# Performance work log

Hardware: AMD Instinct MI355X
Metric: run time of the kernel (lower is better)

Reference implementation:

```python
import jax, jax.numpy as jnp
import numpy as np

LN_EPS = 1e-5
TOP_K = 2

def _layer_norm(x, g, b):
    m = jnp.mean(x, axis=-1, keepdims=True)
    v = jnp.var(x, axis=-1, keepdims=True)
    return (x - m) * jax.lax.rsqrt(v + LN_EPS) * g + b

def _skew(X, pad_value):
    # shift every row one step right: [B,M,L] -> [B,M,M+L]
    B, M, L = X.shape
    X = jnp.pad(X, ((0, 0), (0, 0), (0, M + 1)), constant_values=pad_value)
    X = X.reshape(B, -1)[:, :-M]
    return X.reshape(B, M, M + L)

def _unskew(X):
    # reverse of _skew: [B,M,M+L] -> [B,M,L]
    B, M, Lt = X.shape
    L = Lt - M
    X = X.reshape(B, -1)
    X = jnp.pad(X, ((0, 0), (0, M)))
    return X.reshape(B, M, M + L + 1)[:, :, :L]

def _heads(x, K, D):
    # [B,T,H] -> [B*K,T,D]
    B, T, _ = x.shape
    return x.reshape(B, T, K, D).transpose(0, 2, 1, 3).reshape(B * K, T, D)

def setup_inputs() -> dict:
    key = jax.random.key(0)
    ks = jax.random.split(key, 12)
    B, M, L, H, Dh, E, Kh = 4, 512, 512, 1024, 2048, 8, 8
    D = H // Kh
    s = 0.02
    return {
        "h": jax.random.normal(ks[0], (B, M, H), jnp.float32),
        "h_cache": jax.random.normal(ks[1], (B, L, H), jnp.float32),
        "key_pe": jax.random.normal(ks[2], (1, D, L), jnp.float32) * s,
        "Wq": jax.random.normal(ks[3], (H, H), jnp.float32) * s,
        "Wk": jax.random.normal(ks[4], (H, H), jnp.float32) * s,
        "Wv": jax.random.normal(ks[5], (H, H), jnp.float32) * s,
        "Wo": jax.random.normal(ks[6], (H, H), jnp.float32) * s,
        "ln1_g": jnp.ones((H,), jnp.float32),
        "ln1_b": jnp.zeros((H,), jnp.float32),
        "gate_W": jax.random.normal(ks[7], (H, E), jnp.float32) * s,
        "gate_b": jnp.zeros((E,), jnp.float32),
        "W1": jax.random.normal(ks[8], (E, H, Dh), jnp.float32) * s,
        "b1": jnp.zeros((E, Dh), jnp.float32),
        "W2": jax.random.normal(ks[9], (E, Dh, H), jnp.float32) * s,
        "b2": jnp.zeros((E, H), jnp.float32),
        "ln2_g": jnp.ones((H,), jnp.float32),
        "ln2_b": jnp.zeros((H,), jnp.float32),
    }

def reference(h, h_cache, key_pe, Wq, Wk, Wv, Wo, ln1_g, ln1_b,
              gate_W, gate_b, W1, b1, W2, b2, ln2_g, ln2_b):
    B, M, H = h.shape
    L = h_cache.shape[1]
    Kh = 8
    D = H // Kh
    # --- multi-head relative-position attention over (cache, current) ---
    h_all = jnp.concatenate([h_cache, h], axis=1)            # [B, L+M, H]
    q = _heads(h @ Wq, Kh, D)                                # [B*K, M, D]
    k = _heads(h_all @ Wk, Kh, D)                            # [B*K, M+L, D]
    v = _heads(h_all @ Wv, Kh, D)                            # [B*K, M+L, D]
    attn_cont = _unskew(jnp.einsum('bmd,bnd->bmn', q, k))    # [B*K, M, L]
    attn_pos = jnp.einsum('bmd,xdl->bml', q, key_pe)         # [B*K, M, L]
    attn = jax.nn.softmax((attn_cont + attn_pos) / jnp.sqrt(jnp.float32(D)), axis=-1)
    out = jnp.einsum('bmn,bnd->bmd', _skew(attn, 0.0), v)    # [B*K, M, D]
    out = out.reshape(B, Kh, M, D).transpose(0, 2, 1, 3).reshape(B, M, H)
    attn_out = out @ Wo
    h1 = _layer_norm(h + attn_out, ln1_g, ln1_b)             # post-LN residual
    # --- top-k gated MoE FFN (NaiveGate), post-LN residual ---
    x = h1.reshape(-1, H)                                    # [N, H]
    N = x.shape[0]
    E = gate_b.shape[0]
    logits = x @ gate_W + gate_b                             # [N, E]
    top_val, top_idx = jax.lax.top_k(logits, TOP_K)          # [N, k]
    scores = jax.nn.softmax(top_val, axis=-1)                # [N, k]
    combine = jnp.zeros((N, E), x.dtype).at[jnp.arange(N)[:, None], top_idx].add(scores)
    he = jax.nn.relu(jnp.einsum('nh,ehf->enf', x, W1) + b1[:, None, :])  # [E, N, Dh]
    ye = jnp.einsum('enf,efh->enh', he, W2) + b2[:, None, :]             # [E, N, H]
    core = jnp.einsum('ne,enh->nh', combine, ye).reshape(B, M, H)
    output = _layer_norm(h1 + core, ln2_g, ln2_b)
    return output, top_idx
```

## Files before the change

### kernel.cpp

```cpp
#include <hip/hip_runtime.h>
#include <hip/hip_bf16.h>
#include <stdint.h>


typedef _Float16 f16;
typedef _Float16 f16x8 __attribute__((ext_vector_type(8)));
typedef _Float16 f16x4 __attribute__((ext_vector_type(4)));
typedef float    f32x4 __attribute__((ext_vector_type(4)));
typedef int      i32x4 __attribute__((ext_vector_type(4)));

#define MFMA16(a, b, c) __builtin_amdgcn_mfma_f32_16x16x32_f16((a), (b), (c), 0, 0, 0)
#define LO_SCALE 2048.0f
#define LO_INV   4.8828125e-4f

__device__ __forceinline__ void split2(float x, f16* h, f16* l) {
  f16 hh = (f16)x;
  *h = hh;
  *l = (f16)((x - (float)hh) * LO_SCALE);
}

__device__ __forceinline__ f32x4 zero4() {
  f32x4 z; z[0] = 0.f; z[1] = 0.f; z[2] = 0.f; z[3] = 0.f; return z;
}

__device__ __forceinline__ void gload_lds16(const void* g, void* l) {
  __builtin_amdgcn_global_load_lds((__attribute__((address_space(1))) void*)g,
                                   (__attribute__((address_space(3))) void*)l,
                                   16, 0, 0);
}

__global__ void __launch_bounds__(256) cast_hall_k(const float* __restrict__ h,
                                                   const float* __restrict__ hc,
                                                   f16* __restrict__ hi,
                                                   f16* __restrict__ lo) {
  int c = blockIdx.x * 256 + threadIdx.x;
  int e0 = c * 8;
  int row = e0 >> 10;
  int col = e0 & 1023;
  int b = row >> 10, pos = row & 1023;
  const float* src = (pos < 512) ? (hc + (size_t)((b << 9) + pos) * 1024 + col)
                                 : (h  + (size_t)((b << 9) + (pos - 512)) * 1024 + col);
  float4 v0 = ((const float4*)src)[0];
  float4 v1 = ((const float4*)src)[1];
  float xs[8] = {v0.x, v0.y, v0.z, v0.w, v1.x, v1.y, v1.z, v1.w};
  f16x8 vh, vl;
#pragma unroll
  for (int i = 0; i < 8; i++) { f16 a, bb; split2(xs[i], &a, &bb); vh[i] = a; vl[i] = bb; }
  *(f16x8*)&hi[e0] = vh;
  *(f16x8*)&lo[e0] = vl;
}

template <int SPLIT>
__global__ void __launch_bounds__(256) transpose_cast_k(const float* __restrict__ in,
                                                        f16* __restrict__ oh,
                                                        f16* __restrict__ ol,
                                                        int R, int C) {
  in += (size_t)blockIdx.z * R * C;
  oh += (size_t)blockIdx.z * R * C;
  if constexpr (SPLIT) ol += (size_t)blockIdx.z * R * C;
  __shared__ float tile[32][33];
  int c0 = blockIdx.x * 32, r0 = blockIdx.y * 32;
  int tr = threadIdx.x >> 3, tc = (threadIdx.x & 7) * 4;
  float4 v = *(const float4*)&in[(size_t)(r0 + tr) * C + c0 + tc];
  tile[tr][tc + 0] = v.x; tile[tr][tc + 1] = v.y; tile[tr][tc + 2] = v.z; tile[tr][tc + 3] = v.w;
  __syncthreads();
  int oc = tr;
  int orr = tc;
  f16x4 vh, vl;
#pragma unroll
  for (int i = 0; i < 4; i++) {
    float x = tile[orr + i][oc];
    f16 a, bb; split2(x, &a, &bb);
    vh[i] = a; vl[i] = bb;
  }
  *(f16x4*)&oh[(size_t)(c0 + oc) * R + r0 + orr] = vh;
  if constexpr (SPLIT) *(f16x4*)&ol[(size_t)(c0 + oc) * R + r0 + orr] = vl;
}

#define AM_ID 0
#define AM_GA 2
#define AM_PA 3
#define EP_QKV 0
#define EP_F32 2
#define EP_HE 3
#define EP_YE 4

template <int SPLIT, int BM, int BN, int AMAP, int EPI>
__global__ void __launch_bounds__(256) gemm_k(
    const f16* __restrict__ Ah, const f16* __restrict__ Al,
    const f16* __restrict__ Bh, const f16* __restrict__ Bl,
    void* __restrict__ o0, void* __restrict__ o1,
    const float* __restrict__ bias,
    int Kd, int strideA, int bExpStride,
    const int* __restrict__ list, const int* __restrict__ bases,
    const int* __restrict__ counts) {
  constexpr int PL = SPLIT ? 2 : 1;
  constexpr int MT = BM / 32;
  constexpr int NT = BN / 32;
  constexpr int AIT = BM / 64;
  constexpr int BIT = BN / 64;
  const int e = blockIdx.z;
  int cnt = 0, base0 = 0;
  if constexpr (AMAP == AM_GA || AMAP == AM_PA) {
    cnt = counts[e]; base0 = bases[e];
    if ((int)blockIdx.y * BM >= cnt) return;
    Bh += (size_t)e * bExpStride;
  }
  __shared__ f16 sA[PL][BM * 32];
  __shared__ f16 sB[PL][BN * 32];
  const int n0 = blockIdx.x * BN, r0 = blockIdx.y * BM;
  const int tid = threadIdx.x, lane = tid & 63, wv = tid >> 6;
  const int wm = (wv >> 1) * (BM / 2), wn = (wv & 1) * (BN / 2);

  f32x4 accM[MT][NT], accC[MT][NT];
#pragma unroll
  for (int i = 0; i < MT; i++)
#pragma unroll
    for (int j = 0; j < NT; j++) { accM[i][j] = zero4(); accC[i][j] = zero4(); }

  int aRow[AIT], aCu[AIT];
#pragma unroll
  for (int c = 0; c < AIT; c++) {
    int u = c * 256 + tid;
    int r = u >> 2, cu = u & 3;
    aCu[c] = ((cu ^ ((r >> 1) & 3)) << 3);
    int rr = r0 + r;
    int g;
    if constexpr (AMAP == AM_ID) g = rr;
    else if constexpr (AMAP == AM_GA) g = (rr < cnt) ? list[base0 + rr] : 0;
    else g = base0 + rr;
    aRow[c] = g;
  }
  int bRow[BIT], bCu[BIT];
#pragma unroll
  for (int c = 0; c < BIT; c++) {
    int u = c * 256 + tid;
    int r = u >> 2, cu = u & 3;
    bCu[c] = ((cu ^ ((r >> 1) & 3)) << 3);
    bRow[c] = n0 + r;
  }

  for (int k0 = 0; k0 < Kd; k0 += 32) {
#pragma unroll
    for (int c = 0; c < AIT; c++) {
      int u = c * 256 + tid;
      gload_lds16(&Ah[(size_t)aRow[c] * strideA + k0 + aCu[c]], &sA[0][u * 8]);
      if constexpr (SPLIT)
        gload_lds16(&Al[(size_t)aRow[c] * strideA + k0 + aCu[c]], &sA[1][u * 8]);
    }
#pragma unroll
    for (int c = 0; c < BIT; c++) {
      int u = c * 256 + tid;
      gload_lds16(&Bh[(size_t)bRow[c] * Kd + k0 + bCu[c]], &sB[0][u * 8]);
      if constexpr (SPLIT)
        gload_lds16(&Bl[(size_t)bRow[c] * Kd + k0 + bCu[c]], &sB[1][u * 8]);
    }
    __syncthreads();

    f16x8 ah[MT], al[MT];
#pragma unroll
    for (int mt = 0; mt < MT; mt++) {
      int r = wm + mt * 16 + (lane & 15);
      int cu = (lane >> 4) ^ ((r >> 1) & 3);
      ah[mt] = *(const f16x8*)&sA[0][(r * 4 + cu) * 8];
      if constexpr (SPLIT) al[mt] = *(const f16x8*)&sA[1][(r * 4 + cu) * 8];
    }
#pragma unroll
    for (int nt = 0; nt < NT; nt++) {
      int r = wn + nt * 16 + (lane & 15);
      int cu = (lane >> 4) ^ ((r >> 1) & 3);
      f16x8 bh = *(const f16x8*)&sB[0][(r * 4 + cu) * 8];
      f16x8 bl;
      if constexpr (SPLIT) bl = *(const f16x8*)&sB[1][(r * 4 + cu) * 8];
#pragma unroll
      for (int mt = 0; mt < MT; mt++) {
        accM[mt][nt] = MFMA16(ah[mt], bh, accM[mt][nt]);
        if constexpr (SPLIT) {
          accC[mt][nt] = MFMA16(ah[mt], bl, accC[mt][nt]);
          accC[mt][nt] = MFMA16(al[mt], bh, accC[mt][nt]);
        }
      }
    }
    __syncthreads();
  }

#pragma unroll
  for (int mt = 0; mt < MT; mt++)
#pragma unroll
    for (int nt = 0; nt < NT; nt++)
#pragma unroll
      for (int rg = 0; rg < 4; rg++) {
        int row = r0 + wm + mt * 16 + ((lane >> 4) << 2) + rg;
        int col = n0 + wn + nt * 16 + (lane & 15);
        float v = accM[mt][nt][rg];
        if constexpr (SPLIT) v += accC[mt][nt][rg] * LO_INV;
        if constexpr (EPI == EP_QKV) {
          f16* QH = (f16*)o0;
          f16* QL = QH + (1u << 21);
          f16* KH = QL + (1u << 21);
          f16* KL = KH + (1u << 22);
          f16* VTH = KL + (1u << 22);
          f16* VTL = VTH + (1u << 22);
          int b = row >> 10, pos = row & 1023;
          int seg = col >> 10, hd = (col >> 7) & 7, d = col & 127;
          f16 hh, ll; split2(v, &hh, &ll);
          if (seg == 0) {
            if (pos >= 512) {
              size_t ad = ((size_t)((((b << 3) + hd) << 9) + (pos - 512))) * 128 + d;
              QH[ad] = hh; QL[ad] = ll;
            }
          } else if (seg == 1) {
            size_t ad = ((size_t)((((b << 3) + hd) << 10) + pos)) * 128 + d;
            KH[ad] = hh; KL[ad] = ll;
          } else {
            size_t ad = ((size_t)((((b << 3) + hd) << 7) + d)) * 1024 + pos;
            VTH[ad] = hh; VTL[ad] = ll;
          }
        } else if constexpr (EPI == EP_F32) {
          ((float*)o0)[(size_t)row * 1024 + col] = v;
        } else if constexpr (EPI == EP_HE) {
          if (row < cnt) {
            float t = v + bias[(e << 11) + col];
            ((f16*)o0)[(size_t)(base0 + row) * 2048 + col] = (f16)fmaxf(t, 0.f);
          }
        } else if constexpr (EPI == EP_YE) {
          if (row < cnt)
            ((float*)o0)[(size_t)(base0 + row) * 1024 + col] = v + bias[(e << 10) + col];
        }
      }
}

__device__ __forceinline__ void unpack_p(const unsigned* sp, f16x8* hi, f16x8* lo) {
  i32x4 u0 = *(const i32x4*)sp;
  i32x4 u1 = *(const i32x4*)(sp + 4);
  i32x4 h, l;
  h[0] = (u0[0] & 0xffff) | (u0[1] << 16);
  h[1] = (u0[2] & 0xffff) | (u0[3] << 16);
  h[2] = (u1[0] & 0xffff) | (u1[1] << 16);
  h[3] = (u1[2] & 0xffff) | (u1[3] << 16);
  l[0] = (int)(((unsigned)u0[0] >> 16) | ((unsigned)u0[1] & 0xffff0000u));
  l[1] = (int)(((unsigned)u0[2] >> 16) | ((unsigned)u0[3] & 0xffff0000u));
  l[2] = (int)(((unsigned)u1[0] >> 16) | ((unsigned)u1[1] & 0xffff0000u));
  l[3] = (int)(((unsigned)u1[2] >> 16) | ((unsigned)u1[3] & 0xffff0000u));
  *hi = __builtin_bit_cast(f16x8, h);
  *lo = __builtin_bit_cast(f16x8, l);
}

__global__ void __launch_bounds__(256) attn_k(
    const f16* __restrict__ qh_, const f16* __restrict__ ql_,
    const f16* __restrict__ kh_, const f16* __restrict__ kl_,
    const f16* __restrict__ ph_, const f16* __restrict__ pl_,
    const f16* __restrict__ vh_, const f16* __restrict__ vl_,
    f16* __restrict__ oh_, f16* __restrict__ ol_) {
  __shared__ float S[32][548];
  const int bh = blockIdx.y;
  const int m0 = blockIdx.x * 32;
  const int tid = threadIdx.x, lane = tid & 63, wv = tid >> 6;
  const int lr = lane & 15, lgp = lane >> 4;

  f16x8 qh[2][4], ql[2][4];
  {
    const size_t qbase = ((size_t)bh * 512 + m0) * 128;
#pragma unroll
    for (int mt = 0; mt < 2; mt++)
#pragma unroll
      for (int kb = 0; kb < 4; kb++) {
        size_t off = qbase + (size_t)(mt * 16 + lr) * 128 + kb * 32 + lgp * 8;
        qh[mt][kb] = *(const f16x8*)&qh_[off];
        ql[mt][kb] = *(const f16x8*)&ql_[off];
      }
  }

  {
    const size_t kbase = ((size_t)bh * 1024 + m0) * 128;
    int ntB = (wv < 2) ? wv * 9 : 18 + (wv - 2) * 8;
    int ntE = ntB + ((wv < 2) ? 9 : 8);
    for (int nt = ntB; nt < ntE; ++nt) {
      f16x8 kh[4], kl[4];
#pragma unroll
      for (int kb = 0; kb < 4; kb++) {
        size_t off = kbase + (size_t)(nt * 16 + lr) * 128 + kb * 32 + lgp * 8;
        kh[kb] = *(const f16x8*)&kh_[off];
        kl[kb] = *(const f16x8*)&kl_[off];
      }
      f32x4 aM[2], aC[2];
      aM[0] = zero4(); aM[1] = zero4(); aC[0] = zero4(); aC[1] = zero4();
#pragma unroll
      for (int kb = 0; kb < 4; kb++)
#pragma unroll
        for (int mt = 0; mt < 2; mt++) {
          aM[mt] = MFMA16(qh[mt][kb], kh[kb], aM[mt]);
          aC[mt] = MFMA16(qh[mt][kb], kl[kb], aC[mt]);
          aC[mt] = MFMA16(ql[mt][kb], kh[kb], aC[mt]);
        }
#pragma unroll
      for (int mt = 0; mt < 2; mt++)
#pragma unroll
        for (int rg = 0; rg < 4; rg++) {
          int m = mt * 16 + lgp * 4 + rg;
          S[m][nt * 16 + lr] = aM[mt][rg] + aC[mt][rg] * LO_INV;
        }
    }
  }
  __syncthreads();

  {
    for (int lt = wv * 8; lt < wv * 8 + 8; ++lt) {
      f16x8 eh[4], el[4];
#pragma unroll
      for (int kb = 0; kb < 4; kb++) {
        size_t off = (size_t)(lt * 16 + lr) * 128 + kb * 32 + lgp * 8;
        eh[kb] = *(const f16x8*)&ph_[off];
        el[kb] = *(const f16x8*)&pl_[off];
      }
      f32x4 aM[2], aC[2];
      aM[0] = zero4(); aM[1] = zero4(); aC[0] = zero4(); aC[1] = zero4();
#pragma unroll
      for (int kb = 0; kb < 4; kb++)
#pragma unroll
        for (int mt = 0; mt < 2; mt++) {
          aM[mt] = MFMA16(qh[mt][kb], eh[kb], aM[mt]);
          aC[mt] = MFMA16(qh[mt][kb], el[kb], aC[mt]);
          aC[mt] = MFMA16(ql[mt][kb], eh[kb], aC[mt]);
        }
#pragma unroll
      for (int mt = 0; mt < 2; mt++)
#pragma unroll
        for (int rg = 0; rg < 4; rg++) {
          int m = mt * 16 + lgp * 4 + rg;
          int lc = lt * 16 + lr;
          S[m][m + lc] += aM[mt][rg] + aC[mt][rg] * LO_INV;
        }
    }
  }
  __syncthreads();

  {
    const float scl = 0.08838834764831843f;
    for (int rr = 0; rr < 8; ++rr) {
      int m = wv * 8 + rr;
      float mx = -3.0e38f;
#pragma unroll
      for (int it = 0; it < 9; ++it) {
        int j = it * 64 + lane;
        if (j < 544 && j >= m && j < m + 512) mx = fmaxf(mx, S[m][j]);
      }
#pragma unroll
      for (int o = 32; o > 0; o >>= 1) mx = fmaxf(mx, __shfl_xor(mx, o));
      float pv[9]; float sm = 0.f;
#pragma unroll
      for (int it = 0; it < 9; ++it) {
        int j = it * 64 + lane;
        float p = 0.f;
        if (j < 544 && j >= m && j < m + 512) p = expf((S[m][j] - mx) * scl);
        pv[it] = p; sm += p;
      }
#pragma unroll
      for (int o = 32; o > 0; o >>= 1) sm += __shfl_xor(sm, o);
      float inv = 1.0f / sm;
#pragma unroll
      for (int it = 0; it < 9; ++it) {
        int j = it * 64 + lane;
        if (j < 544) {
          float pn = pv[it] * inv;
          f16 hh, ll; split2(pn, &hh, &ll);
          unsigned pk = (unsigned)__builtin_bit_cast(unsigned short, hh) |
                        ((unsigned)__builtin_bit_cast(unsigned short, ll) << 16);
          ((unsigned*)&S[m][0])[j] = pk;
        }
      }
    }
  }
  __syncthreads();

  f32x4 accM[2][2], accC[2][2];
#pragma unroll
  for (int i = 0; i < 2; i++)
#pragma unroll
    for (int j = 0; j < 2; j++) { accM[i][j] = zero4(); accC[i][j] = zero4(); }
  for (int kb = 0; kb < 17; ++kb) {
    f16x8 pah[2], pal[2];
#pragma unroll
    for (int mt = 0; mt < 2; mt++) {
      const unsigned* sp = (const unsigned*)&S[mt * 16 + lr][0] + kb * 32 + lgp * 8;
      unpack_p(sp, &pah[mt], &pal[mt]);
    }
#pragma unroll
    for (int ntl = 0; ntl < 2; ++ntl) {
      int d = wv * 32 + ntl * 16 + lr;
      size_t off = ((size_t)bh * 128 + d) * 1024 + m0 + kb * 32 + lgp * 8;
      f16x8 vh = *(const f16x8*)&vh_[off];
      f16x8 vl = *(const f16x8*)&vl_[off];
#pragma unroll
      for (int mt = 0; mt < 2; mt++) {
        accM[mt][ntl] = MFMA16(pah[mt], vh, accM[mt][ntl]);
        accC[mt][ntl] = MFMA16(pah[mt], vl, accC[mt][ntl]);
        accC[mt][ntl] = MFMA16(pal[mt], vh, accC[mt][ntl]);
      }
    }
  }
  const int b = bh >> 3, hd = bh & 7;
#pragma unroll
  for (int mt = 0; mt < 2; mt++)
#pragma unroll
    for (int ntl = 0; ntl < 2; ntl++)
#pragma unroll
      for (int rg = 0; rg < 4; rg++) {
        int m = mt * 16 + lgp * 4 + rg;
        int d = wv * 32 + ntl * 16 + lr;
        float v = accM[mt][ntl][rg] + accC[mt][ntl][rg] * LO_INV;
        size_t ad = ((size_t)(b * 512 + m0 + m)) * 1024 + hd * 128 + d;
        f16 hh, ll; split2(v, &hh, &ll);
        oh_[ad] = hh; ol_[ad] = ll;
      }
}

__device__ __forceinline__ float blk_sum(float v, float* red) {
#pragma unroll
  for (int o = 32; o > 0; o >>= 1) v += __shfl_xor(v, o);
  int wv = threadIdx.x >> 6;
  if ((threadIdx.x & 63) == 0) red[wv] = v;
  __syncthreads();
  float r = red[0] + red[1] + red[2] + red[3];
  __syncthreads();
  return r;
}

__global__ void __launch_bounds__(256) ln1_k(const float* __restrict__ h,
                                             const float* __restrict__ ap,
                                             const float* __restrict__ g,
                                             const float* __restrict__ bb,
                                             float* __restrict__ h1,
                                             f16* __restrict__ h1h) {
  int row = blockIdx.x;
  __shared__ float red[4];
  float4 hv = ((const float4*)(h + (size_t)row * 1024))[threadIdx.x];
  float4 av = ((const float4*)(ap + (size_t)row * 1024))[threadIdx.x];
  float4 x; x.x = hv.x + av.x; x.y = hv.y + av.y; x.z = hv.z + av.z; x.w = hv.w + av.w;
  float s = x.x + x.y + x.z + x.w;
  s = blk_sum(s, red);
  float mean = s * (1.0f / 1024.0f);
  float4 d; d.x = x.x - mean; d.y = x.y - mean; d.z = x.z - mean; d.w = x.w - mean;
  float s2 = d.x * d.x + d.y * d.y + d.z * d.z + d.w * d.w;
  s2 = blk_sum(s2, red);
  float var = s2 * (1.0f / 1024.0f);
  float inv = 1.0f / sqrtf(var + 1e-5f);
  float4 gv = ((const float4*)g)[threadIdx.x];
  float4 bv = ((const float4*)bb)[threadIdx.x];
  float4 y; y.x = d.x * inv * gv.x + bv.x; y.y = d.y * inv * gv.y + bv.y;
  y.z = d.z * inv * gv.z + bv.z; y.w = d.w * inv * gv.w + bv.w;
  ((float4*)(h1 + (size_t)row * 1024))[threadIdx.x] = y;
  f16x4 yh; yh[0] = (f16)y.x; yh[1] = (f16)y.y; yh[2] = (f16)y.z; yh[3] = (f16)y.w;
  *(f16x4*)&h1h[(size_t)row * 1024 + threadIdx.x * 4] = yh;
}

__global__ void __launch_bounds__(256) gate_k(const float* __restrict__ h1,
                                              const float* __restrict__ gW,
                                              const float* __restrict__ gb,
                                              float* __restrict__ outIdx,
                                              float* __restrict__ sc,
                                              int* __restrict__ te,
                                              int* __restrict__ ctrl) {
  int t = blockIdx.x * 4 + (threadIdx.x >> 6);
  int lane = threadIdx.x & 63;
  float a0 = 0, a1 = 0, a2 = 0, a3 = 0, a4 = 0, a5 = 0, a6 = 0, a7 = 0;
  for (int i = lane; i < 1024; i += 64) {
    float x = h1[(size_t)t * 1024 + i];
    const float4* w = (const float4*)&gW[i * 8];
    float4 w0 = w[0], w1 = w[1];
    a0 += x * w0.x; a1 += x * w0.y; a2 += x * w0.z; a3 += x * w0.w;
    a4 += x * w1.x; a5 += x * w1.y; a6 += x * w1.z; a7 += x * w1.w;
  }
  float av[8] = {a0, a1, a2, a3, a4, a5, a6, a7};
#pragma unroll
  for (int e = 0; e < 8; e++)
#pragma unroll
    for (int o = 32; o > 0; o >>= 1) av[e] += __shfl_xor(av[e], o);
  if (lane == 0) {
#pragma unroll
    for (int e = 0; e < 8; e++) av[e] += gb[e];
    int i0 = 0; float v0 = av[0];
#pragma unroll
    for (int e = 1; e < 8; e++) if (av[e] > v0) { v0 = av[e]; i0 = e; }
    int i1 = -1; float v1 = -3.0e38f;
#pragma unroll
    for (int e = 0; e < 8; e++) if (e != i0 && av[e] > v1) { v1 = av[e]; i1 = e; }
    float ex = expf(v1 - v0);
    float den = 1.0f + ex;
    outIdx[t * 2] = (float)i0; outIdx[t * 2 + 1] = (float)i1;
    sc[t * 2] = 1.0f / den; sc[t * 2 + 1] = ex / den;
    te[t * 2] = i0; te[t * 2 + 1] = i1;
    atomicAdd(&ctrl[i0], 1); atomicAdd(&ctrl[i1], 1);
  }
}

__global__ void scan_k(int* ctrl) {
  if (threadIdx.x == 0 && blockIdx.x == 0) {
    int s = 0;
    for (int e = 0; e < 8; e++) { ctrl[8 + e] = s; s += ctrl[e]; }
  }
}

__global__ void __launch_bounds__(256) scatter_k(const int* __restrict__ te,
                                                 int* ctrl,
                                                 int* __restrict__ list,
                                                 int* __restrict__ ppos) {
  int t = blockIdx.x * 256 + threadIdx.x;
  if (t >= 2048) return;
#pragma unroll
  for (int s = 0; s < 2; s++) {
    int e = te[t * 2 + s];
    int pos = atomicAdd(&ctrl[16 + e], 1);
    int pr = ctrl[8 + e] + pos;
    list[pr] = t;
    ppos[t * 2 + s] = pr;
  }
}

__global__ void __launch_bounds__(256) comb_ln2_k(const float* __restrict__ h1,
                                                  const float* __restrict__ ye,
                                                  const float* __restrict__ sc,
                                                  const int* __restrict__ ppos,
                                                  const float* __restrict__ g,
                                                  const float* __restrict__ bb,
                                                  float* __restrict__ out) {
  int row = blockIdx.x;
  __shared__ float red[4];
  int p0 = ppos[row * 2], p1 = ppos[row * 2 + 1];
  float s0 = sc[row * 2], s1 = sc[row * 2 + 1];
  float4 a = ((const float4*)(h1 + (size_t)row * 1024))[threadIdx.x];
  float4 y0 = ((const float4*)(ye + (size_t)p0 * 1024))[threadIdx.x];
  float4 y1 = ((const float4*)(ye + (size_t)p1 * 1024))[threadIdx.x];
  float4 x;
  x.x = a.x + s0 * y0.x + s1 * y1.x; x.y = a.y + s0 * y0.y + s1 * y1.y;
  x.z = a.z + s0 * y0.z + s1 * y1.z; x.w = a.w + s0 * y0.w + s1 * y1.w;
  float s = x.x + x.y + x.z + x.w;
  s = blk_sum(s, red);
  float mean = s * (1.0f / 1024.0f);
  float4 d; d.x = x.x - mean; d.y = x.y - mean; d.z = x.z - mean; d.w = x.w - mean;
  float s2 = d.x * d.x + d.y * d.y + d.z * d.z + d.w * d.w;
  s2 = blk_sum(s2, red);
  float var = s2 * (1.0f / 1024.0f);
  float inv = 1.0f / sqrtf(var + 1e-5f);
  float4 gv = ((const float4*)g)[threadIdx.x];
  float4 bv = ((const float4*)bb)[threadIdx.x];
  float4 y; y.x = d.x * inv * gv.x + bv.x; y.y = d.y * inv * gv.y + bv.y;
  y.z = d.z * inv * gv.z + bv.z; y.w = d.w * inv * gv.w + bv.w;
  ((float4*)(out + (size_t)row * 1024))[threadIdx.x] = y;
}

extern "C" void kernel_launch(void* const* d_in, const int* in_sizes, int n_in,
                              void* d_out, int out_size, void* d_ws, size_t ws_size,
                              hipStream_t stream) {
  const float* h   = (const float*)d_in[0];
  const float* hc  = (const float*)d_in[1];
  const float* pe  = (const float*)d_in[2];
  const float* Wq  = (const float*)d_in[3];
  const float* Wk  = (const float*)d_in[4];
  const float* Wv  = (const float*)d_in[5];
  const float* Wo  = (const float*)d_in[6];
  const float* g1  = (const float*)d_in[7];
  const float* b1n = (const float*)d_in[8];
  const float* gW  = (const float*)d_in[9];
  const float* gb  = (const float*)d_in[10];
  const float* W1  = (const float*)d_in[11];
  const float* b1e = (const float*)d_in[12];
  const float* W2  = (const float*)d_in[13];
  const float* b2e = (const float*)d_in[14];
  const float* g2  = (const float*)d_in[15];
  const float* b2n = (const float*)d_in[16];
  float* out = (float*)d_out;
  float* outIdx = out + 2097152;

  char* w = (char*)d_ws;
  size_t off = 0;
  auto alloc = [&](size_t bytes) -> char* {
    char* p = w + off;
    off += (bytes + 255) & ~(size_t)255;
    return p;
  };
  int*   ctrl    = (int*)alloc(128);
  f16*   hallH   = (f16*)alloc(4096ull * 1024 * 2);
  f16*   hallL   = (f16*)alloc(4096ull * 1024 * 2);
  f16*   WqkvtH  = (f16*)alloc(3072ull * 1024 * 2);
  f16*   WqkvtL  = (f16*)alloc(3072ull * 1024 * 2);
  f16*   WotH    = (f16*)alloc(1024ull * 1024 * 2);
  f16*   WotL    = (f16*)alloc(1024ull * 1024 * 2);
  f16*   peH     = (f16*)alloc(512ull * 128 * 2);
  f16*   peL     = (f16*)alloc(512ull * 128 * 2);
  f16*   qkv     = (f16*)alloc(20971520ull * 2);
  f16*   qH  = qkv;
  f16*   qL  = qH + (1u << 21);
  f16*   kH  = qL + (1u << 21);
  f16*   kL  = kH + (1u << 22);
  f16*   vtH = kL + (1u << 22);
  f16*   vtL = vtH + (1u << 22);
  f16*   attH  = (f16*)alloc(2097152ull * 2);
  f16*   attL  = (f16*)alloc(2097152ull * 2);
  float* aproj = (float*)alloc(2097152ull * 4);
  float* h1    = (float*)alloc(2097152ull * 4);
  f16*   h1h   = (f16*)alloc(2097152ull * 2);
  f16*   W1t   = (f16*)alloc(16777216ull * 2);
  f16*   W2t   = (f16*)alloc(16777216ull * 2);
  f16*   he    = (f16*)alloc(4224ull * 2048 * 2);
  float* ye    = (float*)alloc(4224ull * 1024 * 4);
  float* scb   = (float*)alloc(2048ull * 2 * 4);
  int*   te    = (int*)alloc(2048ull * 2 * 4);
  int*   ppos  = (int*)alloc(2048ull * 2 * 4);
  int*   list  = (int*)alloc(4096ull * 4);
  (void)in_sizes; (void)n_in; (void)out_size; (void)ws_size;

  hipMemsetAsync(ctrl, 0, 128, stream);

  cast_hall_k<<<2048, 256, 0, stream>>>(h, hc, hallH, hallL);
  transpose_cast_k<1><<<dim3(32, 32, 1), 256, 0, stream>>>(Wq, WqkvtH, WqkvtL, 1024, 1024);
  transpose_cast_k<1><<<dim3(32, 32, 1), 256, 0, stream>>>(Wk, WqkvtH + 1048576, WqkvtL + 1048576, 1024, 1024);
  transpose_cast_k<1><<<dim3(32, 32, 1), 256, 0, stream>>>(Wv, WqkvtH + 2097152, WqkvtL + 2097152, 1024, 1024);
  transpose_cast_k<1><<<dim3(32, 32, 1), 256, 0, stream>>>(Wo, WotH, WotL, 1024, 1024);
  transpose_cast_k<1><<<dim3(16, 4, 1), 256, 0, stream>>>(pe, peH, peL, 128, 512);
  transpose_cast_k<0><<<dim3(64, 32, 8), 256, 0, stream>>>(W1, W1t, nullptr, 1024, 2048);
  transpose_cast_k<0><<<dim3(32, 64, 8), 256, 0, stream>>>(W2, W2t, nullptr, 2048, 1024);

  gemm_k<1, 128, 64, AM_ID, EP_QKV><<<dim3(48, 32, 1), 256, 0, stream>>>(
      hallH, hallL, WqkvtH, WqkvtL, qkv, nullptr, nullptr, 1024, 1024, 0,
      nullptr, nullptr, nullptr);

  attn_k<<<dim3(16, 32, 1), 256, 0, stream>>>(qH, qL, kH, kL, peH, peL, vtH, vtL, attH, attL);

  gemm_k<1, 64, 64, AM_ID, EP_F32><<<dim3(16, 32, 1), 256, 0, stream>>>(
      attH, attL, WotH, WotL, aproj, nullptr, nullptr, 1024, 1024, 0,
      nullptr, nullptr, nullptr);
  ln1_k<<<2048, 256, 0, stream>>>(h, aproj, g1, b1n, h1, h1h);

  gate_k<<<512, 256, 0, stream>>>(h1, gW, gb, outIdx, scb, te, ctrl);
  scan_k<<<1, 64, 0, stream>>>(ctrl);
  scatter_k<<<8, 256, 0, stream>>>(te, ctrl, list, ppos);

  gemm_k<0, 64, 128, AM_GA, EP_HE><<<dim3(16, 32, 8), 256, 0, stream>>>(
      h1h, nullptr, W1t, nullptr, he, nullptr, b1e, 1024, 1024, 2048 * 1024,
      list, ctrl + 8, ctrl);
  gemm_k<0, 64, 128, AM_PA, EP_YE><<<dim3(8, 32, 8), 256, 0, stream>>>(
      he, nullptr, W2t, nullptr, ye, nullptr, b2e, 2048, 2048, 1024 * 2048,
      nullptr, ctrl + 8, ctrl);

  comb_ln2_k<<<2048, 256, 0, stream>>>(h1, ye, scb, ppos, g2, b2n, out);
}
```

Before: 669.2 us.

## Pre-pack weights into MFMA fragment layout and load B directly to registers

Replaces the weight transpose-cast with a kernel that writes weights in per-lane MFMA B-fragment order (16-column by 32-k blobs). The GEMM then loads B operands straight from global memory into registers, dropping the B shared-memory tile and its LDS reads. This cuts LDS traffic and shared-memory footprint. The cost is that each wave re-reads B from global/L2 without sharing it across the waves that use the same columns, and the loads are not double-buffered.

New measurement: 665.0 us. About the same (-0.6%).

```diff
diff --git a/kernel.cpp b/kernel.cpp
--- a/kernel.cpp
+++ b/kernel.cpp
@@ -48,6 +48,41 @@
   for (int i = 0; i < 8; i++) { f16 a, bb; split2(xs[i], &a, &bb); vh[i] = a; vl[i] = bb; }
   *(f16x8*)&hi[e0] = vh;
   *(f16x8*)&lo[e0] = vl;
+}
+
+template <int SPLIT>
+__global__ void __launch_bounds__(256) wprep_k(const float* __restrict__ in,
+                                               f16* __restrict__ oh,
+                                               f16* __restrict__ ol,
+                                               int K, int N) {
+  in += (size_t)blockIdx.z * K * N;
+  oh += (size_t)blockIdx.z * K * N;
+  if constexpr (SPLIT) ol += (size_t)blockIdx.z * K * N;
+  __shared__ float tile[32][33];
+  const int n0 = blockIdx.x * 32, k0 = blockIdx.y * 32;
+  {
+    int r = threadIdx.x >> 3, c4 = (threadIdx.x & 7) * 4;
+    float4 v = *(const float4*)&in[(size_t)(k0 + r) * N + n0 + c4];
+    tile[r][c4 + 0] = v.x; tile[r][c4 + 1] = v.y;
+    tile[r][c4 + 2] = v.z; tile[r][c4 + 3] = v.w;
+  }
+  __syncthreads();
+  int t = threadIdx.x;
+  if constexpr (!SPLIT) { if (t >= 128) return; }
+  int half = SPLIT ? (t >> 7) : 0;
+  int r = t & 127;
+  int nt = r >> 6, lane = r & 63;
+  int lr = lane & 15, lgp = lane >> 4;
+  f16x8 v;
+#pragma unroll
+  for (int j = 0; j < 8; j++) {
+    float x = tile[lgp * 8 + j][nt * 16 + lr];
+    f16 hh, ll; split2(x, &hh, &ll);
+    v[j] = half ? ll : hh;
+  }
+  size_t blob = (((size_t)(n0 >> 4) + nt) * (K >> 5) + (k0 >> 5)) * 512 + lane * 8;
+  f16* dst = half ? ol : oh;
+  *(f16x8*)&dst[blob] = v;
 }
 
 template <int SPLIT>
@@ -98,19 +133,20 @@
   constexpr int MT = BM / 32;
   constexpr int NT = BN / 32;
   constexpr int AIT = BM / 64;
-  constexpr int BIT = BN / 64;
   const int e = blockIdx.z;
   int cnt = 0, base0 = 0;
   if constexpr (AMAP == AM_GA || AMAP == AM_PA) {
     cnt = counts[e]; base0 = bases[e];
     if ((int)blockIdx.y * BM >= cnt) return;
     Bh += (size_t)e * bExpStride;
+    if constexpr (SPLIT) Bl += (size_t)e * bExpStride;
   }
   __shared__ f16 sA[PL][BM * 32];
-  __shared__ f16 sB[PL][BN * 32];
   const int n0 = blockIdx.x * BN, r0 = blockIdx.y * BM;
   const int tid = threadIdx.x, lane = tid & 63, wv = tid >> 6;
   const int wm = (wv >> 1) * (BM / 2), wn = (wv & 1) * (BN / 2);
+  const int bKt = Kd >> 5;
+  const int gnt0 = (n0 + wn) >> 4;
 
   f32x4 accM[MT][NT], accC[MT][NT];
 #pragma unroll
@@ -131,16 +167,16 @@
     else g = base0 + rr;
     aRow[c] = g;
   }
-  int bRow[BIT], bCu[BIT];
-#pragma unroll
-  for (int c = 0; c < BIT; c++) {
-    int u = c * 256 + tid;
-    int r = u >> 2, cu = u & 3;
-    bCu[c] = ((cu ^ ((r >> 1) & 3)) << 3);
-    bRow[c] = n0 + r;
-  }
 
   for (int k0 = 0; k0 < Kd; k0 += 32) {
+    const int kt = k0 >> 5;
+    f16x8 bh[NT], bl[NT];
+#pragma unroll
+    for (int nt = 0; nt < NT; nt++) {
+      size_t bi = ((size_t)(gnt0 + nt) * bKt + kt) * 512 + lane * 8;
+      bh[nt] = *(const f16x8*)&Bh[bi];
+      if constexpr (SPLIT) bl[nt] = *(const f16x8*)&Bl[bi];
+    }
 #pragma unroll
     for (int c = 0; c < AIT; c++) {
       int u = c * 256 + tid;
@@ -148,13 +184,6 @@
       if constexpr (SPLIT)
         gload_lds16(&Al[(size_t)aRow[c] * strideA + k0 + aCu[c]], &sA[1][u * 8]);
     }
-#pragma unroll
-    for (int c = 0; c < BIT; c++) {
-      int u = c * 256 + tid;
-      gload_lds16(&Bh[(size_t)bRow[c] * Kd + k0 + bCu[c]], &sB[0][u * 8]);
-      if constexpr (SPLIT)
-        gload_lds16(&Bl[(size_t)bRow[c] * Kd + k0 + bCu[c]], &sB[1][u * 8]);
-    }
     __syncthreads();
 
     f16x8 ah[MT], al[MT];
@@ -167,17 +196,12 @@
     }
 #pragma unroll
     for (int nt = 0; nt < NT; nt++) {
-      int r = wn + nt * 16 + (lane & 15);
-      int cu = (lane >> 4) ^ ((r >> 1) & 3);
-      f16x8 bh = *(const f16x8*)&sB[0][(r * 4 + cu) * 8];
-      f16x8 bl;
-      if constexpr (SPLIT) bl = *(const f16x8*)&sB[1][(r * 4 + cu) * 8];
 #pragma unroll
       for (int mt = 0; mt < MT; mt++) {
-        accM[mt][nt] = MFMA16(ah[mt], bh, accM[mt][nt]);
+        accM[mt][nt] = MFMA16(ah[mt], bh[nt], accM[mt][nt]);
         if constexpr (SPLIT) {
-          accC[mt][nt] = MFMA16(ah[mt], bl, accC[mt][nt]);
-          accC[mt][nt] = MFMA16(al[mt], bh, accC[mt][nt]);
+          accC[mt][nt] = MFMA16(ah[mt], bl[nt], accC[mt][nt]);
+          accC[mt][nt] = MFMA16(al[mt], bh[nt], accC[mt][nt]);
         }
       }
     }
@@ -613,13 +637,13 @@
   hipMemsetAsync(ctrl, 0, 128, stream);
 
   cast_hall_k<<<2048, 256, 0, stream>>>(h, hc, hallH, hallL);
-  transpose_cast_k<1><<<dim3(32, 32, 1), 256, 0, stream>>>(Wq, WqkvtH, WqkvtL, 1024, 1024);
-  transpose_cast_k<1><<<dim3(32, 32, 1), 256, 0, stream>>>(Wk, WqkvtH + 1048576, WqkvtL + 1048576, 1024, 1024);
-  transpose_cast_k<1><<<dim3(32, 32, 1), 256, 0, stream>>>(Wv, WqkvtH + 2097152, WqkvtL + 2097152, 1024, 1024);
-  transpose_cast_k<1><<<dim3(32, 32, 1), 256, 0, stream>>>(Wo, WotH, WotL, 1024, 1024);
+  wprep_k<1><<<dim3(32, 32, 1), 256, 0, stream>>>(Wq, WqkvtH, WqkvtL, 1024, 1024);
+  wprep_k<1><<<dim3(32, 32, 1), 256, 0, stream>>>(Wk, WqkvtH + 1048576, WqkvtL + 1048576, 1024, 1024);
+  wprep_k<1><<<dim3(32, 32, 1), 256, 0, stream>>>(Wv, WqkvtH + 2097152, WqkvtL + 2097152, 1024, 1024);
+  wprep_k<1><<<dim3(32, 32, 1), 256, 0, stream>>>(Wo, WotH, WotL, 1024, 1024);
   transpose_cast_k<1><<<dim3(16, 4, 1), 256, 0, stream>>>(pe, peH, peL, 128, 512);
-  transpose_cast_k<0><<<dim3(64, 32, 8), 256, 0, stream>>>(W1, W1t, nullptr, 1024, 2048);
-  transpose_cast_k<0><<<dim3(32, 64, 8), 256, 0, stream>>>(W2, W2t, nullptr, 2048, 1024);
+  wprep_k<0><<<dim3(64, 32, 8), 256, 0, stream>>>(W1, W1t, nullptr, 1024, 2048);
+  wprep_k<0><<<dim3(32, 64, 8), 256, 0, stream>>>(W2, W2t, nullptr, 2048, 1024);
 
   gemm_k<1, 128, 64, AM_ID, EP_QKV><<<dim3(48, 32, 1), 256, 0, stream>>>(
       hallH, hallL, WqkvtH, WqkvtL, qkv, nullptr, nullptr, 1024, 1024, 0,
```
